# Performance work log

Hardware: AMD Instinct MI355X
Metric: run time of the kernel (lower is better)

The kernel has to match this reference:

```python
import jax, jax.numpy as jnp
import numpy as np

L, N, E, H = 1024, 8, 1024, 8


def setup_inputs() -> dict:
    key = jax.random.key(0)
    ks = jax.random.split(key, 9)
    s = 0.02
    return {
        "query": jax.random.normal(ks[0], (L, N, E), jnp.float32),
        "key": jax.random.normal(ks[1], (L, N, E), jnp.float32),
        "value": jax.random.normal(ks[2], (L, N, E), jnp.float32),
        "Wqkv": jax.random.normal(ks[3], (H, 3 * E, E), jnp.float32) * s,
        "bqkv": jax.random.normal(ks[4], (H, 3 * E), jnp.float32) * s,
        "Wo": jax.random.normal(ks[5], (H, E, E), jnp.float32) * s,
        "bo": jax.random.normal(ks[6], (H, E), jnp.float32) * s,
        "Wout": jax.random.normal(ks[7], (E, H * E), jnp.float32) * s,
        "bout": jax.random.normal(ks[8], (E,), jnp.float32) * s,
    }


def reference(query, key, value, Wqkv, bqkv, Wo, bo, Wout, bout):
    # Each of H independent single-head MultiheadAttention modules, batched over h.
    Wq, Wk, Wv = Wqkv[:, :E], Wqkv[:, E:2 * E], Wqkv[:, 2 * E:]   # [H,E,E] each
    bq, bk, bv = bqkv[:, :E], bqkv[:, E:2 * E], bqkv[:, 2 * E:]   # [H,E]
    # Projections: (L,N,E) x (H,E,E) -> (H,L,N,E)
    q = jnp.einsum('lne,hde->hlnd', query, Wq) + bq[:, None, None, :]
    k = jnp.einsum('sne,hde->hsnd', key, Wk) + bk[:, None, None, :]
    v = jnp.einsum('sne,hde->hsnd', value, Wv) + bv[:, None, None, :]
    scale = 1.0 / jnp.sqrt(jnp.asarray(E, q.dtype))  # head_dim == E since 1 head per module
    scores = jnp.einsum('hlnd,hsnd->hnls', q, k) * scale  # [H,N,L,S]
    attn_weights = jax.nn.softmax(scores, axis=-1)
    ctx = jnp.einsum('hnls,hsnd->hlnd', attn_weights, v)   # [H,L,N,E]
    head_out = jnp.einsum('hlnd,hed->hlne', ctx, Wo) + bo[:, None, None, :]
    # concat along last dim: (L,N,H*E)
    concat = jnp.transpose(head_out, (1, 2, 0, 3)).reshape(L, N, H * E)
    out = concat @ Wout.T + bout  # (L,N,E)
    return out, attn_weights  # weights: [H,N,L,S] (stack of per-head (N,L,S))
```

## Files before the change

kernel.cpp:

```cpp
#include <hip/hip_runtime.h>
#include <stdint.h>


typedef unsigned short u16;
typedef unsigned int u32;
typedef __attribute__((ext_vector_type(8))) __bf16 bf16x8;
typedef __attribute__((ext_vector_type(4))) float f32x4;
typedef __attribute__((ext_vector_type(4))) u16 u16x4;

#define DEVFN static __device__ __forceinline__

static constexpr int LQ = 1024, NN = 8, EE = 1024, HH = 8, SS = 1024;
static constexpr long LNE = (long)LQ * NN * EE;
static constexpr long MM = 1048576;

static constexpr long OF_QBF   = 0;
static constexpr long OF_KBF   = 8388608;
static constexpr long OF_VALT  = 16777216;
static constexpr long OF_F     = 25165824;
static constexpr long OF_WKT   = 33554432;
static constexpr long OF_WVT   = 41943040;
static constexpr long OF_WOT   = 50331648;
static constexpr long OF_WOUTB = 58720256;
static constexpr long OF_GT    = 67108864;
static constexpr long OF_BM    = 75497472;
static constexpr long OF_T     = 83886080;
static constexpr long OF_U     = 150994944;
static constexpr long OF_PART_F  = 109051904;
static constexpr long OF_SMALL_F = 125829120;

DEVFN u16 f2bf(float x) {
  u32 u = __builtin_bit_cast(u32, x);
  u = (u + 0x7FFFu + ((u >> 16) & 1u)) >> 16;
  return (u16)u;
}
DEVFN float bf2f(u16 x) { return __builtin_bit_cast(float, (u32)x << 16); }

DEVFN void gload16(const u16* g, u16* l) {
  __builtin_amdgcn_global_load_lds(
      (const __attribute__((address_space(1))) void*)(uintptr_t)g,
      (__attribute__((address_space(3))) void*)(uintptr_t)l, 16, 0, 0);
}

struct Cvt3P { const float* s[3]; u16* d[3]; };
__global__ __launch_bounds__(256) void k_cvt3(Cvt3P p) {
  const int z = blockIdx.y;
  const float* s = p.s[z];
  u16* d = p.d[z];
  long i = (long)blockIdx.x * 256 + threadIdx.x;
  for (; i < 2097152; i += 131072) {
    float4 v = reinterpret_cast<const float4*>(s)[i];
    u16x4 o;
    o.x = f2bf(v.x); o.y = f2bf(v.y); o.z = f2bf(v.z); o.w = f2bf(v.w);
    reinterpret_cast<u16x4*>(d)[i] = o;
  }
}

struct Tp5P { const float* s[5]; u16* d[5]; int sld[5]; long szs[5]; long dzs[5]; };
__global__ __launch_bounds__(256) void k_tp5(Tp5P p) {
  const int cfg = blockIdx.z >> 3, zz = blockIdx.z & 7;
  const float* src = p.s[cfg] + (long)zz * p.szs[cfg];
  u16* dst = p.d[cfg] + (long)zz * p.dzs[cfg];
  const int sld = p.sld[cfg];
  __shared__ float t[64][65];
  const int r = threadIdx.x >> 4, c4 = (threadIdx.x & 15) * 4;
#pragma unroll
  for (int rr = 0; rr < 64; rr += 16) {
    float4 v = *reinterpret_cast<const float4*>(
        &src[(long)(blockIdx.y * 64 + r + rr) * sld + blockIdx.x * 64 + c4]);
    t[r + rr][c4] = v.x; t[r + rr][c4 + 1] = v.y;
    t[r + rr][c4 + 2] = v.z; t[r + rr][c4 + 3] = v.w;
  }
  __syncthreads();
#pragma unroll
  for (int rr = 0; rr < 64; rr += 16) {
    u16x4 o;
    o.x = f2bf(t[c4][r + rr]);     o.y = f2bf(t[c4 + 1][r + rr]);
    o.z = f2bf(t[c4 + 2][r + rr]); o.w = f2bf(t[c4 + 3][r + rr]);
    *reinterpret_cast<u16x4*>(
        &dst[(long)(blockIdx.x * 64 + r + rr) * 1024 + blockIdx.y * 64 + c4]) = o;
  }
}

__global__ __launch_bounds__(256) void k_c(const float* __restrict__ bqkv,
                                           float* __restrict__ c) {
  const int h = blockIdx.x, t = threadIdx.x;
  float s = 0.f;
  for (int i = t; i < 1024; i += 256)
    s += bqkv[h * 3072 + i] * bqkv[h * 3072 + 1024 + i];
#pragma unroll
  for (int o = 1; o < 64; o <<= 1) s += __shfl_xor(s, o);
  __shared__ float ps[4];
  if ((t & 63) == 0) ps[t >> 6] = s;
  __syncthreads();
  if (t == 0) c[h] = ps[0] + ps[1] + ps[2] + ps[3];
}

__global__ __launch_bounds__(256) void k_ab(const float* __restrict__ Wqkv,
                                            const float* __restrict__ bqkv,
                                            float* __restrict__ ap,
                                            float* __restrict__ bp) {
  const int ec = blockIdx.x, h = blockIdx.y, dc = blockIdx.z, t = threadIdx.x;
  const int e = ec * 256 + t;
  const float* wq = Wqkv + (long)h * 3145728;
  const float* wk = wq + 1048576;
  const float* bq = bqkv + h * 3072;
  const float* bk = bq + 1024;
  float sa = 0.f, sb = 0.f;
  for (int dd = 0; dd < 128; ++dd) {
    const int d = dc * 128 + dd;
    sa += wq[(long)d * 1024 + e] * bk[d];
    sb += wk[(long)d * 1024 + e] * bq[d];
  }
  ap[dc * 8192 + h * 1024 + e] = sa;
  bp[dc * 8192 + h * 1024 + e] = sb;
}

__global__ __launch_bounds__(256) void k_red(const float* __restrict__ ap,
                                             const float* __restrict__ bp,
                                             float* __restrict__ a,
                                             float* __restrict__ b) {
  const int i = blockIdx.x * 256 + threadIdx.x;
  float sa = 0.f, sb = 0.f;
#pragma unroll
  for (int dc = 0; dc < 8; ++dc) { sa += ap[dc * 8192 + i]; sb += bp[dc * 8192 + i]; }
  a[i] = sa; b[i] = sb;
}

__global__ __launch_bounds__(256) void k_rowdot(const float* __restrict__ X,
                                                const float* __restrict__ V,
                                                const float* __restrict__ c,
                                                float* __restrict__ OUT,
                                                int addc) {
  const int wave = threadIdx.x >> 6, lane = threadIdx.x & 63;
  const int r = blockIdx.x * 4 + wave;
  const float4* xr = reinterpret_cast<const float4*>(X + (long)r * 1024);
  float acc[8];
#pragma unroll
  for (int h = 0; h < 8; ++h) acc[h] = 0.f;
#pragma unroll
  for (int it = 0; it < 4; ++it) {
    float4 q = xr[it * 64 + lane];
#pragma unroll
    for (int h = 0; h < 8; ++h) {
      float4 av = reinterpret_cast<const float4*>(V + h * 1024)[it * 64 + lane];
      acc[h] += q.x * av.x + q.y * av.y + q.z * av.z + q.w * av.w;
    }
  }
#pragma unroll
  for (int h = 0; h < 8; ++h)
#pragma unroll
    for (int o = 1; o < 64; o <<= 1) acc[h] += __shfl_xor(acc[h], o);
  if (lane == 0) {
    const int idx = r >> 3, n = r & 7;
#pragma unroll
    for (int h = 0; h < 8; ++h)
      OUT[h * 8192 + n * 1024 + idx] = acc[h] + (addc ? c[h] : 0.f);
  }
}

__global__ __launch_bounds__(256) void k_be2(const float* __restrict__ Wout,
                                             const float* __restrict__ bo,
                                             const float* __restrict__ bout,
                                             const float* __restrict__ bqkv,
                                             const u16* __restrict__ Bm,
                                             float* __restrict__ be2) {
  const int e = blockIdx.x, t = threadIdx.x;
  float s = 0.f;
  for (int i = t; i < 8192; i += 256) {
    s += Wout[(long)e * 8192 + i] * bo[i];
    const int h = i >> 10, d = i & 1023;
    s += bf2f(Bm[(long)e * 8192 + i]) * bqkv[h * 3072 + 2048 + d];
  }
#pragma unroll
  for (int o = 1; o < 64; o <<= 1) s += __shfl_xor(s, o);
  __shared__ float ps[4];
  if ((t & 63) == 0) ps[t >> 6] = s;
  __syncthreads();
  if (t == 0) be2[e] = bout[e] + ps[0] + ps[1] + ps[2] + ps[3];
}

__global__ __launch_bounds__(256) void k_combine(const float* __restrict__ p0,
                                                 const float* __restrict__ p1,
                                                 const float* __restrict__ be,
                                                 float* __restrict__ out) {
  long i = (long)blockIdx.x * 256 + threadIdx.x;
  const long st = (long)gridDim.x * 256;
  for (; i < 2097152; i += st) {
    float4 a = reinterpret_cast<const float4*>(p0)[i];
    float4 b = reinterpret_cast<const float4*>(p1)[i];
    float4 c = reinterpret_cast<const float4*>(be)[i & 255];
    float4 o = {a.x + b.x + c.x, a.y + b.y + c.y, a.z + b.z + c.z, a.w + b.w + c.w};
    reinterpret_cast<float4*>(out)[i] = o;
  }
}

__global__ __launch_bounds__(256) void k_softmax(float* __restrict__ S,
                                                 u16* __restrict__ P) {
  __shared__ float smax[4], ssum[4];
  const long row = blockIdx.x;
  float* sr = S + row * 1024;
  const int tid = threadIdx.x;
  float4 v = reinterpret_cast<const float4*>(sr)[tid];
  float m = fmaxf(fmaxf(v.x, v.y), fmaxf(v.z, v.w));
#pragma unroll
  for (int o = 1; o < 64; o <<= 1) m = fmaxf(m, __shfl_xor(m, o));
  const int wv = tid >> 6, ln = tid & 63;
  if (ln == 0) smax[wv] = m;
  __syncthreads();
  m = fmaxf(fmaxf(smax[0], smax[1]), fmaxf(smax[2], smax[3]));
  v.x = __expf(v.x - m); v.y = __expf(v.y - m);
  v.z = __expf(v.z - m); v.w = __expf(v.w - m);
  float s = v.x + v.y + v.z + v.w;
#pragma unroll
  for (int o = 1; o < 64; o <<= 1) s += __shfl_xor(s, o);
  if (ln == 0) ssum[wv] = s;
  __syncthreads();
  s = ssum[0] + ssum[1] + ssum[2] + ssum[3];
  const float inv = 1.0f / s;
  v.x *= inv; v.y *= inv; v.z *= inv; v.w *= inv;
  reinterpret_cast<float4*>(sr)[tid] = v;
  u16x4 o4;
  o4.x = f2bf(v.x); o4.y = f2bf(v.y); o4.z = f2bf(v.z); o4.w = f2bf(v.w);
  reinterpret_cast<u16x4*>(P + row * 1024)[tid] = o4;
}

struct GemmP {
  const u16* A; const u16* B;
  const float* bR; const float* bC;
  float* Cf; u16* Cb;
  int lda, ldb, ldc, K, NB;
  long sAh, sAn, sBh, sBn, sCh, sCn;
  long bRh, bRn, bCh, bCn;
  float scale;
};
struct GemmP2 { GemmP p0, p1; int split; };

template <int M0, int N0>
DEVFN void quad(f32x4 (&acc)[8][4], bf16x8 (&a)[4][2], bf16x8 (&b)[4][2]) {
#pragma unroll
  for (int mi = 0; mi < 4; ++mi)
#pragma unroll
    for (int ni = 0; ni < 2; ++ni) {
      acc[M0 + mi][N0 + ni] = __builtin_amdgcn_mfma_f32_16x16x32_bf16(
          a[mi][0], b[N0 + ni][0], acc[M0 + mi][N0 + ni], 0, 0, 0);
      acc[M0 + mi][N0 + ni] = __builtin_amdgcn_mfma_f32_16x16x32_bf16(
          a[mi][1], b[N0 + ni][1], acc[M0 + mi][N0 + ni], 0, 0, 0);
    }
}

#define BAR() asm volatile("s_barrier" ::: "memory")
#define VMCNT2() asm volatile("s_waitcnt vmcnt(2)" ::: "memory")
#define VMCNT0() asm volatile("s_waitcnt vmcnt(0)" ::: "memory")
#define SB0() __builtin_amdgcn_sched_barrier(0)

DEVFN void swz_block(int& bx, int& by, int& bz) {
  long lid = blockIdx.x + (long)gridDim.x * (blockIdx.y + (long)gridDim.y * blockIdx.z);
  const long nwg = (long)gridDim.x * gridDim.y * gridDim.z;
  long s = (nwg % 8 == 0) ? ((lid % 8) * (nwg / 8) + lid / 8) : lid;
  bx = (int)(s % gridDim.x);
  long r2 = s / gridDim.x;
  by = (int)(r2 % gridDim.y);
  bz = (int)(r2 / gridDim.y);
}

template <int HAS_BR, int HAS_BC, int OUT_F32>
DEVFN void gemm_body(const GemmP& p, int bx, int by, int bz) {
  const int h = bz / p.NB, n = bz % p.NB;
  const u16* Ab = p.A + (long)h * p.sAh + (long)n * p.sAn;
  const u16* Bb = p.B + (long)h * p.sBh + (long)n * p.sBn;
  const long coff = (long)h * p.sCh + (long)n * p.sCn;
  const int row0 = by * 256;
  const int col0 = bx * 256;

  __shared__ u16 LDSU[65536];

  const int tid = threadIdx.x;
  const int wave = tid >> 6, lane = tid & 63;
  const int wr = wave >> 2, wc = wave & 3;
  const int NT = p.K >> 6;

  f32x4 acc[8][4];
  const f32x4 zero = {0.f, 0.f, 0.f, 0.f};
#pragma unroll
  for (int i = 0; i < 8; ++i)
#pragma unroll
    for (int j = 0; j < 4; ++j) acc[i][j] = zero;

  const int swc = ((lane & 7) ^ ((lane >> 3) & 7)) * 8;
  const u16* Ag = Ab + (long)(row0 + wave * 16 + (lane >> 3)) * p.lda + swc;
  const u16* Bg = Bb + (long)(col0 + wave * 16 + (lane >> 3)) * p.ldb + swc;

  auto STAGE = [&](int hh) {
    const int kt = hh >> 2;
    if (kt < NT) {
      const int pt = hh & 3;
      const int hf = pt >> 1;
      u16* l = &LDSU[((pt & 1) ? 32768 : 0) + (kt & 1) * 16384 + hf * 8192 + wave * 1024];
      const int ld = (pt & 1) ? p.ldb : p.lda;
      const u16* g = ((pt & 1) ? Bg : Ag) + (long)hf * 128 * ld + kt * 64;
      gload16(g, l);
      gload16(g + 8L * ld, l + 512);
    }
  };

  STAGE(0); STAGE(1); STAGE(2); STAGE(3); STAGE(4);
  VMCNT2();
  BAR();

  const int rA = lane & 15;
  const int c0 = (((lane >> 4)) ^ (lane & 7)) * 8;
  const int c1 = ((4 + (lane >> 4)) ^ (lane & 7)) * 8;

  bf16x8 a[4][2], b[4][2];

  for (int t = 0; t < NT; ++t) {
    const int db = (t & 1) * 16384;
    const u16* Ar = &LDSU[db + wr * 8192 + rA * 64];
    const u16* Br = &LDSU[32768 + db + (wc >> 1) * 8192 + ((wc & 1) * 64 + rA) * 64];

#pragma unroll
    for (int mi = 0; mi < 4; ++mi) {
      a[mi][0] = *reinterpret_cast<const bf16x8*>(&Ar[mi * 1024 + c0]);
      a[mi][1] = *reinterpret_cast<const bf16x8*>(&Ar[mi * 1024 + c1]);
    }
#pragma unroll
    for (int ni = 0; ni < 2; ++ni) {
      b[ni][0] = *reinterpret_cast<const bf16x8*>(&Br[ni * 1024 + c0]);
      b[ni][1] = *reinterpret_cast<const bf16x8*>(&Br[ni * 1024 + c1]);
    }
    STAGE(4 * t + 5);
    BAR();
    SB0(); __builtin_amdgcn_s_setprio(1);
    quad<0, 0>(acc, a, b);
    __builtin_amdgcn_s_setprio(0); SB0();
    BAR();

#pragma unroll
    for (int ni = 2; ni < 4; ++ni) {
      b[ni][0] = *reinterpret_cast<const bf16x8*>(&Br[ni * 1024 + c0]);
      b[ni][1] = *reinterpret_cast<const bf16x8*>(&Br[ni * 1024 + c1]);
    }
    STAGE(4 * t + 6);
    BAR();
    SB0(); __builtin_amdgcn_s_setprio(1);
    quad<0, 2>(acc, a, b);
    __builtin_amdgcn_s_setprio(0); SB0();
    BAR();

#pragma unroll
    for (int mi = 0; mi < 4; ++mi) {
      a[mi][0] = *reinterpret_cast<const bf16x8*>(&Ar[(4 + mi) * 1024 + c0]);
      a[mi][1] = *reinterpret_cast<const bf16x8*>(&Ar[(4 + mi) * 1024 + c1]);
    }
    STAGE(4 * t + 7);
    BAR();
    SB0(); __builtin_amdgcn_s_setprio(1);
    quad<4, 0>(acc, a, b);
    __builtin_amdgcn_s_setprio(0); SB0();
    BAR();

    STAGE(4 * t + 8);
    if (t < NT - 2) { VMCNT2(); }
    else if (t == NT - 2) { VMCNT0(); }
    BAR();
    SB0(); __builtin_amdgcn_s_setprio(1);
    quad<4, 2>(acc, a, b);
    __builtin_amdgcn_s_setprio(0); SB0();
    BAR();
  }

  const int crow = (lane >> 4) * 4;
  const int ccol = lane & 15;
#pragma unroll
  for (int mi = 0; mi < 8; ++mi) {
#pragma unroll
    for (int j = 0; j < 4; ++j) {
      const int grow = row0 + wr * 128 + mi * 16 + crow + j;
#pragma unroll
      for (int ni = 0; ni < 4; ++ni) {
        const int gcol = col0 + wc * 64 + ni * 16 + ccol;
        float v = acc[mi][ni][j];
        if constexpr (HAS_BR) v += p.bR[(long)h * p.bRh + (long)n * p.bRn + grow];
        if constexpr (HAS_BC) v += p.bC[(long)h * p.bCh + (long)n * p.bCn + gcol];
        v *= p.scale;
        if constexpr (OUT_F32)
          p.Cf[coff + (long)grow * p.ldc + gcol] = v;
        else
          p.Cb[coff + (long)grow * p.ldc + gcol] = f2bf(v);
      }
    }
  }
}

template <int HAS_BR, int HAS_BC, int OUT_F32>
__global__ __launch_bounds__(512, 2) void k_gemm256(GemmP p) {
  int bx, by, bz;
  swz_block(bx, by, bz);
  gemm_body<HAS_BR, HAS_BC, OUT_F32>(p, bx, by, bz);
}

template <int HAS_BR, int HAS_BC, int OUT_F32>
__global__ __launch_bounds__(512, 2) void k_gemm256_pair(GemmP2 pp) {
  int bx, by, bz;
  swz_block(bx, by, bz);
  if (bz < pp.split)
    gemm_body<HAS_BR, HAS_BC, OUT_F32>(pp.p0, bx, by, bz);
  else
    gemm_body<HAS_BR, HAS_BC, OUT_F32>(pp.p1, bx, by, bz - pp.split);
}

extern "C" void kernel_launch(void* const* d_in, const int* in_sizes, int n_in,
                              void* d_out, int out_size, void* d_ws,
                              size_t ws_size, hipStream_t stream) {
  const float* query = (const float*)d_in[0];
  const float* key_  = (const float*)d_in[1];
  const float* value = (const float*)d_in[2];
  const float* Wqkv  = (const float*)d_in[3];
  const float* bqkv  = (const float*)d_in[4];
  const float* Wo    = (const float*)d_in[5];
  const float* bo    = (const float*)d_in[6];
  const float* Wout  = (const float*)d_in[7];
  const float* bout  = (const float*)d_in[8];

  float* out  = (float*)d_out;
  float* attn = out + LNE;

  u16* ws = (u16*)d_ws;
  u16* qbf   = ws + OF_QBF;
  u16* kbf   = ws + OF_KBF;
  u16* valT  = ws + OF_VALT;
  u16* WqT_F = ws + OF_F;
  u16* WkT   = ws + OF_WKT;
  u16* WvT   = ws + OF_WVT;
  u16* WoT   = ws + OF_WOT;
  u16* Woutb = ws + OF_WOUTB;
  u16* Gt    = ws + OF_GT;
  u16* Bm    = ws + OF_BM;
  u16* Tbuf  = ws + OF_T;
  u16* Ubuf  = ws + OF_U;
  float* part = (float*)d_ws + OF_PART_F;
  float* S    = (float*)d_ws + OF_SMALL_F;
  float* av    = S;
  float* bv2   = S + 8192;
  float* cc    = S + 16384;
  float* alpha = S + 16400;
  float* beta  = S + 81936;
  float* be2   = S + 147472;
  float* apart = S + 148496;
  float* bpart = S + 214032;

  {
    Cvt3P p;
    p.s[0] = query; p.s[1] = key_; p.s[2] = Wout;
    p.d[0] = qbf;   p.d[1] = kbf;  p.d[2] = Woutb;
    k_cvt3<<<dim3(512, 3), 256, 0, stream>>>(p);
  }
  {
    Tp5P p;
    p.s[0] = Wqkv;           p.d[0] = WqT_F; p.sld[0] = 1024; p.szs[0] = 3145728; p.dzs[0] = MM;
    p.s[1] = Wqkv + 1048576; p.d[1] = WkT;   p.sld[1] = 1024; p.szs[1] = 3145728; p.dzs[1] = MM;
    p.s[2] = Wqkv + 2097152; p.d[2] = WvT;   p.sld[2] = 1024; p.szs[2] = 3145728; p.dzs[2] = MM;
    p.s[3] = Wo;             p.d[3] = WoT;   p.sld[3] = 1024; p.szs[3] = MM;      p.dzs[3] = MM;
    p.s[4] = value;          p.d[4] = valT;  p.sld[4] = 8192; p.szs[4] = 1024;    p.dzs[4] = MM;
    k_tp5<<<dim3(16, 16, 40), 256, 0, stream>>>(p);
  }
  k_c<<<8, 256, 0, stream>>>(bqkv, cc);
  k_ab<<<dim3(4, 8, 8), 256, 0, stream>>>(Wqkv, bqkv, apart, bpart);
  k_red<<<32, 256, 0, stream>>>(apart, bpart, av, bv2);
  k_rowdot<<<2048, 256, 0, stream>>>(query, av, cc, alpha, 1);
  k_rowdot<<<2048, 256, 0, stream>>>(key_, bv2, cc, beta, 0);

  const dim3 blk(512);

  {
    GemmP g = {};
    g.A = WkT; g.lda = 1024; g.sAh = MM; g.sAn = 0;
    g.B = WqT_F; g.ldb = 1024; g.sBh = MM; g.sBn = 0;
    g.Cb = Gt; g.ldc = 1024; g.sCh = MM; g.sCn = 0;
    g.K = 1024; g.NB = 1; g.scale = 1.f;
    GemmP m = {};
    m.A = Woutb; m.lda = 8192; m.sAh = 1024; m.sAn = 0;
    m.B = WoT; m.ldb = 1024; m.sBh = MM; m.sBn = 0;
    m.Cb = Bm; m.ldc = 8192; m.sCh = 1024; m.sCn = 0;
    m.K = 1024; m.NB = 1; m.scale = 1.f;
    GemmP2 pp = {g, m, 8};
    k_gemm256_pair<0, 0, 0><<<dim3(4, 4, 16), blk, 0, stream>>>(pp);
  }
  k_be2<<<1024, 256, 0, stream>>>(Wout, bo, bout, bqkv, Bm, be2);
  {
    GemmP t = {};
    t.A = qbf; t.lda = 8192; t.sAh = 0; t.sAn = 1024;
    t.B = Gt; t.ldb = 1024; t.sBh = MM; t.sBn = 0;
    t.Cb = Tbuf; t.ldc = 8192; t.sCh = 8388608; t.sCn = 1024;
    t.K = 1024; t.NB = 8; t.scale = 1.f;
    GemmP f = {};
    f.A = Bm; f.lda = 8192; f.sAh = 1024; f.sAn = 0;
    f.B = WvT; f.ldb = 1024; f.sBh = MM; f.sBn = 0;
    f.Cb = WqT_F; f.ldc = 8192; f.sCh = 1024; f.sCn = 0;
    f.K = 1024; f.NB = 1; f.scale = 1.f;
    GemmP2 pp = {t, f, 64};
    k_gemm256_pair<0, 0, 0><<<dim3(4, 4, 72), blk, 0, stream>>>(pp);
  }
  {
    GemmP p = {};
    p.A = Tbuf; p.lda = 8192; p.sAh = 8388608; p.sAn = 1024;
    p.B = kbf; p.ldb = 8192; p.sBh = 0; p.sBn = 1024;
    p.Cf = attn; p.ldc = 1024; p.sCh = 8388608; p.sCn = 1048576;
    p.bR = alpha; p.bRh = 8192; p.bRn = 1024;
    p.bC = beta;  p.bCh = 8192; p.bCn = 1024;
    p.K = 1024; p.NB = 8; p.scale = 1.f / 32.f;
    k_gemm256<1, 1, 1><<<dim3(4, 4, 64), blk, 0, stream>>>(p);
  }
  k_softmax<<<HH * NN * LQ, 256, 0, stream>>>(attn, Tbuf);
  {
    GemmP p = {};
    p.A = Tbuf; p.lda = 1024; p.sAh = 8388608; p.sAn = 1048576;
    p.B = valT; p.ldb = 1024; p.sBh = 0; p.sBn = 1048576;
    p.Cb = Ubuf; p.ldc = 65536; p.sCh = 1024; p.sCn = 8192;
    p.K = 1024; p.NB = 8; p.scale = 1.f;
    k_gemm256<0, 0, 0><<<dim3(4, 4, 64), blk, 0, stream>>>(p);
  }
  {
    GemmP p = {};
    p.A = Ubuf; p.lda = 8192; p.sAh = 4096; p.sAn = 0;
    p.B = WqT_F; p.ldb = 8192; p.sBh = 4096; p.sBn = 0;
    p.Cf = part; p.ldc = 1024; p.sCh = 8388608; p.sCn = 0;
    p.K = 4096; p.NB = 1; p.scale = 1.f;
    k_gemm256<0, 0, 1><<<dim3(4, 32, 2), blk, 0, stream>>>(p);
  }
  k_combine<<<2048, 256, 0, stream>>>(part, part + 8388608, be2, out);
}
```

Baseline: 1.004 ms.

## Fuse score GEMM with full-row softmax and drop row-constant bias terms

```diff
diff --git a/kernel.cpp b/kernel.cpp
--- a/kernel.cpp
+++ b/kernel.cpp
@@ -25,9 +25,8 @@
 static constexpr long OF_GT    = 67108864;
 static constexpr long OF_BM    = 75497472;
 static constexpr long OF_T     = 83886080;
-static constexpr long OF_U     = 150994944;
-static constexpr long OF_PART_F  = 109051904;
-static constexpr long OF_SMALL_F = 125829120;
+static constexpr long OF_P     = 150994944;
+static constexpr long OF_SMALL_F = 109051904;
 
 DEVFN u16 f2bf(float x) {
   u32 u = __builtin_bit_cast(u32, x);
@@ -41,6 +40,13 @@
       (const __attribute__((address_space(1))) void*)(uintptr_t)g,
       (__attribute__((address_space(3))) void*)(uintptr_t)l, 16, 0, 0);
 }
+
+#define BAR() asm volatile("s_barrier" ::: "memory")
+#define VMCNT2() asm volatile("s_waitcnt vmcnt(2)" ::: "memory")
+#define VMCNT0() asm volatile("s_waitcnt vmcnt(0)" ::: "memory")
+#define VMCNT8() asm volatile("s_waitcnt vmcnt(8)" ::: "memory")
+#define VMCNT9() asm volatile("s_waitcnt vmcnt(9)" ::: "memory")
+#define SB0() __builtin_amdgcn_sched_barrier(0)
 
 struct Cvt3P { const float* s[3]; u16* d[3]; };
 __global__ __launch_bounds__(256) void k_cvt3(Cvt3P p) {
@@ -82,56 +88,32 @@
   }
 }
 
-__global__ __launch_bounds__(256) void k_c(const float* __restrict__ bqkv,
-                                           float* __restrict__ c) {
-  const int h = blockIdx.x, t = threadIdx.x;
-  float s = 0.f;
-  for (int i = t; i < 1024; i += 256)
-    s += bqkv[h * 3072 + i] * bqkv[h * 3072 + 1024 + i];
-#pragma unroll
-  for (int o = 1; o < 64; o <<= 1) s += __shfl_xor(s, o);
-  __shared__ float ps[4];
-  if ((t & 63) == 0) ps[t >> 6] = s;
-  __syncthreads();
-  if (t == 0) c[h] = ps[0] + ps[1] + ps[2] + ps[3];
-}
-
-__global__ __launch_bounds__(256) void k_ab(const float* __restrict__ Wqkv,
-                                            const float* __restrict__ bqkv,
-                                            float* __restrict__ ap,
-                                            float* __restrict__ bp) {
+__global__ __launch_bounds__(256) void k_bvec(const float* __restrict__ Wqkv,
+                                              const float* __restrict__ bqkv,
+                                              float* __restrict__ bp) {
   const int ec = blockIdx.x, h = blockIdx.y, dc = blockIdx.z, t = threadIdx.x;
   const int e = ec * 256 + t;
-  const float* wq = Wqkv + (long)h * 3145728;
-  const float* wk = wq + 1048576;
+  const float* wk = Wqkv + (long)h * 3145728 + 1048576;
   const float* bq = bqkv + h * 3072;
-  const float* bk = bq + 1024;
-  float sa = 0.f, sb = 0.f;
+  float sb = 0.f;
   for (int dd = 0; dd < 128; ++dd) {
     const int d = dc * 128 + dd;
-    sa += wq[(long)d * 1024 + e] * bk[d];
     sb += wk[(long)d * 1024 + e] * bq[d];
   }
-  ap[dc * 8192 + h * 1024 + e] = sa;
   bp[dc * 8192 + h * 1024 + e] = sb;
 }
-
-__global__ __launch_bounds__(256) void k_red(const float* __restrict__ ap,
-                                             const float* __restrict__ bp,
-                                             float* __restrict__ a,
-                                             float* __restrict__ b) {
+__global__ __launch_bounds__(256) void k_redb(const float* __restrict__ bp,
+                                              float* __restrict__ b) {
   const int i = blockIdx.x * 256 + threadIdx.x;
-  float sa = 0.f, sb = 0.f;
-#pragma unroll
-  for (int dc = 0; dc < 8; ++dc) { sa += ap[dc * 8192 + i]; sb += bp[dc * 8192 + i]; }
-  a[i] = sa; b[i] = sb;
+  float sb = 0.f;
+#pragma unroll
+  for (int dc = 0; dc < 8; ++dc) sb += bp[dc * 8192 + i];
+  b[i] = sb;
 }
 
 __global__ __launch_bounds__(256) void k_rowdot(const float* __restrict__ X,
                                                 const float* __restrict__ V,
-                                                const float* __restrict__ c,
-                                                float* __restrict__ OUT,
-                                                int addc) {
+                                                float* __restrict__ OUT) {
   const int wave = threadIdx.x >> 6, lane = threadIdx.x & 63;
   const int r = blockIdx.x * 4 + wave;
   const float4* xr = reinterpret_cast<const float4*>(X + (long)r * 1024);
@@ -154,8 +136,7 @@
   if (lane == 0) {
     const int idx = r >> 3, n = r & 7;
 #pragma unroll
-    for (int h = 0; h < 8; ++h)
-      OUT[h * 8192 + n * 1024 + idx] = acc[h] + (addc ? c[h] : 0.f);
+    for (int h = 0; h < 8; ++h) OUT[h * 8192 + n * 1024 + idx] = acc[h];
   }
 }
 
@@ -180,58 +161,28 @@
   if (t == 0) be2[e] = bout[e] + ps[0] + ps[1] + ps[2] + ps[3];
 }
 
-__global__ __launch_bounds__(256) void k_combine(const float* __restrict__ p0,
-                                                 const float* __restrict__ p1,
-                                                 const float* __restrict__ be,
-                                                 float* __restrict__ out) {
+__global__ __launch_bounds__(256) void k_combine4(const float* __restrict__ pt,
+                                                  const float* __restrict__ be,
+                                                  float* __restrict__ out) {
   long i = (long)blockIdx.x * 256 + threadIdx.x;
   const long st = (long)gridDim.x * 256;
   for (; i < 2097152; i += st) {
-    float4 a = reinterpret_cast<const float4*>(p0)[i];
-    float4 b = reinterpret_cast<const float4*>(p1)[i];
-    float4 c = reinterpret_cast<const float4*>(be)[i & 255];
-    float4 o = {a.x + b.x + c.x, a.y + b.y + c.y, a.z + b.z + c.z, a.w + b.w + c.w};
+    float4 a = reinterpret_cast<const float4*>(pt)[i];
+    float4 b = reinterpret_cast<const float4*>(pt + 8388608)[i];
+    float4 cc = reinterpret_cast<const float4*>(pt + 16777216)[i];
+    float4 d = reinterpret_cast<const float4*>(pt + 25165824)[i];
+    float4 e = reinterpret_cast<const float4*>(be)[i & 255];
+    float4 o = {a.x + b.x + cc.x + d.x + e.x, a.y + b.y + cc.y + d.y + e.y,
+                a.z + b.z + cc.z + d.z + e.z, a.w + b.w + cc.w + d.w + e.w};
     reinterpret_cast<float4*>(out)[i] = o;
   }
-}
-
-__global__ __launch_bounds__(256) void k_softmax(float* __restrict__ S,
-                                                 u16* __restrict__ P) {
-  __shared__ float smax[4], ssum[4];
-  const long row = blockIdx.x;
-  float* sr = S + row * 1024;
-  const int tid = threadIdx.x;
-  float4 v = reinterpret_cast<const float4*>(sr)[tid];
-  float m = fmaxf(fmaxf(v.x, v.y), fmaxf(v.z, v.w));
-#pragma unroll
-  for (int o = 1; o < 64; o <<= 1) m = fmaxf(m, __shfl_xor(m, o));
-  const int wv = tid >> 6, ln = tid & 63;
-  if (ln == 0) smax[wv] = m;
-  __syncthreads();
-  m = fmaxf(fmaxf(smax[0], smax[1]), fmaxf(smax[2], smax[3]));
-  v.x = __expf(v.x - m); v.y = __expf(v.y - m);
-  v.z = __expf(v.z - m); v.w = __expf(v.w - m);
-  float s = v.x + v.y + v.z + v.w;
-#pragma unroll
-  for (int o = 1; o < 64; o <<= 1) s += __shfl_xor(s, o);
-  if (ln == 0) ssum[wv] = s;
-  __syncthreads();
-  s = ssum[0] + ssum[1] + ssum[2] + ssum[3];
-  const float inv = 1.0f / s;
-  v.x *= inv; v.y *= inv; v.z *= inv; v.w *= inv;
-  reinterpret_cast<float4*>(sr)[tid] = v;
-  u16x4 o4;
-  o4.x = f2bf(v.x); o4.y = f2bf(v.y); o4.z = f2bf(v.z); o4.w = f2bf(v.w);
-  reinterpret_cast<u16x4*>(P + row * 1024)[tid] = o4;
 }
 
 struct GemmP {
   const u16* A; const u16* B;
-  const float* bR; const float* bC;
   float* Cf; u16* Cb;
   int lda, ldb, ldc, K, NB;
   long sAh, sAn, sBh, sBn, sCh, sCn;
-  long bRh, bRn, bCh, bCn;
   float scale;
 };
 struct GemmP2 { GemmP p0, p1; int split; };
@@ -248,11 +199,6 @@
           a[mi][1], b[N0 + ni][1], acc[M0 + mi][N0 + ni], 0, 0, 0);
     }
 }
-
-#define BAR() asm volatile("s_barrier" ::: "memory")
-#define VMCNT2() asm volatile("s_waitcnt vmcnt(2)" ::: "memory")
-#define VMCNT0() asm volatile("s_waitcnt vmcnt(0)" ::: "memory")
-#define SB0() __builtin_amdgcn_sched_barrier(0)
 
 DEVFN void swz_block(int& bx, int& by, int& bz) {
   long lid = blockIdx.x + (long)gridDim.x * (blockIdx.y + (long)gridDim.y * blockIdx.z);
@@ -264,7 +210,7 @@
   bz = (int)(r2 / gridDim.y);
 }
 
-template <int HAS_BR, int HAS_BC, int OUT_F32>
+template <int OUT_F32>
 DEVFN void gemm_body(const GemmP& p, int bx, int by, int bz) {
   const int h = bz / p.NB, n = bz % p.NB;
   const u16* Ab = p.A + (long)h * p.sAh + (long)n * p.sAn;
@@ -380,10 +326,7 @@
 #pragma unroll
       for (int ni = 0; ni < 4; ++ni) {
         const int gcol = col0 + wc * 64 + ni * 16 + ccol;
-        float v = acc[mi][ni][j];
-        if constexpr (HAS_BR) v += p.bR[(long)h * p.bRh + (long)n * p.bRn + grow];
-        if constexpr (HAS_BC) v += p.bC[(long)h * p.bCh + (long)n * p.bCn + gcol];
-        v *= p.scale;
+        float v = acc[mi][ni][j] * p.scale;
         if constexpr (OUT_F32)
           p.Cf[coff + (long)grow * p.ldc + gcol] = v;
         else
@@ -393,21 +336,207 @@
   }
 }
 
-template <int HAS_BR, int HAS_BC, int OUT_F32>
+template <int OUT_F32>
 __global__ __launch_bounds__(512, 2) void k_gemm256(GemmP p) {
   int bx, by, bz;
   swz_block(bx, by, bz);
-  gemm_body<HAS_BR, HAS_BC, OUT_F32>(p, bx, by, bz);
-}
-
-template <int HAS_BR, int HAS_BC, int OUT_F32>
+  gemm_body<OUT_F32>(p, bx, by, bz);
+}
+template <int OUT_F32>
 __global__ __launch_bounds__(512, 2) void k_gemm256_pair(GemmP2 pp) {
   int bx, by, bz;
   swz_block(bx, by, bz);
-  if (bz < pp.split)
-    gemm_body<HAS_BR, HAS_BC, OUT_F32>(pp.p0, bx, by, bz);
-  else
-    gemm_body<HAS_BR, HAS_BC, OUT_F32>(pp.p1, bx, by, bz - pp.split);
+  if (bz < pp.split) gemm_body<OUT_F32>(pp.p0, bx, by, bz);
+  else gemm_body<OUT_F32>(pp.p1, bx, by, bz - pp.split);
+}
+
+struct FscP {
+  const u16* T; const u16* K; const float* beta;
+  float* attn; u16* P;
+};
+__global__ __launch_bounds__(512, 2) void k_fsc(FscP p) {
+  int bx, by, bz;
+  swz_block(bx, by, bz);
+  const int h = by >> 3, n = by & 7;
+  const int row0 = bx * 64;
+
+  __shared__ u16 Abuf[2][64][64];
+  __shared__ u16 Bbuf[2][8][128][32];
+  __shared__ float red[2][64][8];
+
+  const int tid = threadIdx.x;
+  const int w = tid >> 6, lane = tid & 63;
+  const int rl = lane & 15, g = lane >> 4;
+
+  const u16* Abase = p.T + (long)h * 8388608 + n * 1024 + (long)row0 * 8192;
+  const u16* Bbase = p.K + n * 1024;
+  const float* betap = p.beta + h * 8192 + n * 1024 + w * 128 + rl;
+
+  float betv[8];
+#pragma unroll
+  for (int ni = 0; ni < 8; ++ni) betv[ni] = betap[ni * 16];
+
+  f32x4 acc[4][8];
+  const f32x4 zero = {0.f, 0.f, 0.f, 0.f};
+#pragma unroll
+  for (int mi = 0; mi < 4; ++mi)
+#pragma unroll
+    for (int ni = 0; ni < 8; ++ni) acc[mi][ni] = zero;
+
+  const u16* Bg = Bbase + (long)(w * 128 + (lane >> 2)) * 8192 +
+                  ((lane & 3) ^ ((lane >> 2) & 3)) * 8;
+  const u16* Ag = Abase + (long)(w * 8 + (lane >> 3)) * 8192 +
+                  ((lane & 7) ^ ((lane >> 3) & 7)) * 8;
+
+  auto STAGE_B = [&](int j) {
+    u16* l = &Bbuf[j & 1][w][0][0];
+    const u16* gp = Bg + (long)j * 32;
+#pragma unroll
+    for (int i = 0; i < 8; ++i) gload16(gp + (long)i * 16 * 8192, l + i * 512);
+  };
+  auto STAGE_A = [&](int pp2) {
+    gload16(Ag + (long)pp2 * 64, &Abuf[pp2 & 1][w * 8][0]);
+  };
+
+  STAGE_B(0); STAGE_A(0); STAGE_B(1); STAGE_A(1);
+
+  const int cA0 = ((g) ^ (lane & 7)) * 8;
+  const int cA1 = ((4 + g) ^ (lane & 7)) * 8;
+  const int cB = (g ^ (lane & 3)) * 8;
+
+  for (int t2 = 0; t2 < 16; ++t2) {
+    const int pb = t2 & 1;
+    VMCNT9();
+    BAR();
+    {
+      bf16x8 aF[4], bF[8];
+#pragma unroll
+      for (int mi = 0; mi < 4; ++mi)
+        aF[mi] = *reinterpret_cast<const bf16x8*>(&Abuf[pb][mi * 16 + rl][cA0]);
+#pragma unroll
+      for (int ni = 0; ni < 8; ++ni)
+        bF[ni] = *reinterpret_cast<const bf16x8*>(&Bbuf[0][w][ni * 16 + rl][cB]);
+      SB0(); __builtin_amdgcn_s_setprio(1);
+#pragma unroll
+      for (int mi = 0; mi < 4; ++mi)
+#pragma unroll
+        for (int ni = 0; ni < 8; ++ni)
+          acc[mi][ni] = __builtin_amdgcn_mfma_f32_16x16x32_bf16(
+              aF[mi], bF[ni], acc[mi][ni], 0, 0, 0);
+      __builtin_amdgcn_s_setprio(0); SB0();
+    }
+    BAR();
+    if (t2 < 15) STAGE_B(2 * t2 + 2);
+    VMCNT8();
+    BAR();
+    {
+      bf16x8 aF[4], bF[8];
+#pragma unroll
+      for (int mi = 0; mi < 4; ++mi)
+        aF[mi] = *reinterpret_cast<const bf16x8*>(&Abuf[pb][mi * 16 + rl][cA1]);
+#pragma unroll
+      for (int ni = 0; ni < 8; ++ni)
+        bF[ni] = *reinterpret_cast<const bf16x8*>(&Bbuf[1][w][ni * 16 + rl][cB]);
+      SB0(); __builtin_amdgcn_s_setprio(1);
+#pragma unroll
+      for (int mi = 0; mi < 4; ++mi)
+#pragma unroll
+        for (int ni = 0; ni < 8; ++ni)
+          acc[mi][ni] = __builtin_amdgcn_mfma_f32_16x16x32_bf16(
+              aF[mi], bF[ni], acc[mi][ni], 0, 0, 0);
+      __builtin_amdgcn_s_setprio(0); SB0();
+    }
+    BAR();
+    if (t2 < 15) STAGE_B(2 * t2 + 3);
+    if (t2 < 14) STAGE_A(t2 + 2);
+  }
+
+  float rmax[4][4];
+#pragma unroll
+  for (int mi = 0; mi < 4; ++mi)
+#pragma unroll
+    for (int j = 0; j < 4; ++j) {
+      float m = -3.0e38f;
+#pragma unroll
+      for (int ni = 0; ni < 8; ++ni) {
+        float v = (acc[mi][ni][j] + betv[ni]) * 0.03125f;
+        acc[mi][ni][j] = v;
+        m = fmaxf(m, v);
+      }
+      rmax[mi][j] = m;
+    }
+#pragma unroll
+  for (int msk = 1; msk < 16; msk <<= 1)
+#pragma unroll
+    for (int mi = 0; mi < 4; ++mi)
+#pragma unroll
+      for (int j = 0; j < 4; ++j)
+        rmax[mi][j] = fmaxf(rmax[mi][j], __shfl_xor(rmax[mi][j], msk));
+  if (rl == 0) {
+#pragma unroll
+    for (int mi = 0; mi < 4; ++mi)
+#pragma unroll
+      for (int j = 0; j < 4; ++j) red[0][mi * 16 + g * 4 + j][w] = rmax[mi][j];
+  }
+  __syncthreads();
+  float gmax[4][4];
+#pragma unroll
+  for (int mi = 0; mi < 4; ++mi)
+#pragma unroll
+    for (int j = 0; j < 4; ++j) {
+      const int row = mi * 16 + g * 4 + j;
+      float4 x = *reinterpret_cast<const float4*>(&red[0][row][0]);
+      float4 y = *reinterpret_cast<const float4*>(&red[0][row][4]);
+      gmax[mi][j] = fmaxf(fmaxf(fmaxf(x.x, x.y), fmaxf(x.z, x.w)),
+                          fmaxf(fmaxf(y.x, y.y), fmaxf(y.z, y.w)));
+    }
+  float rsum[4][4];
+#pragma unroll
+  for (int mi = 0; mi < 4; ++mi)
+#pragma unroll
+    for (int j = 0; j < 4; ++j) {
+      float s = 0.f;
+#pragma unroll
+      for (int ni = 0; ni < 8; ++ni) {
+        float e = __expf(acc[mi][ni][j] - gmax[mi][j]);
+        acc[mi][ni][j] = e;
+        s += e;
+      }
+      rsum[mi][j] = s;
+    }
+#pragma unroll
+  for (int msk = 1; msk < 16; msk <<= 1)
+#pragma unroll
+    for (int mi = 0; mi < 4; ++mi)
+#pragma unroll
+      for (int j = 0; j < 4; ++j) rsum[mi][j] += __shfl_xor(rsum[mi][j], msk);
+  if (rl == 0) {
+#pragma unroll
+    for (int mi = 0; mi < 4; ++mi)
+#pragma unroll
+      for (int j = 0; j < 4; ++j) red[1][mi * 16 + g * 4 + j][w] = rsum[mi][j];
+  }
+  __syncthreads();
+  float* attn_b = p.attn + ((long)h * 8 + n) * 1048576;
+  u16* P_b = p.P + ((long)h * 8 + n) * 1048576;
+#pragma unroll
+  for (int mi = 0; mi < 4; ++mi)
+#pragma unroll
+    for (int j = 0; j < 4; ++j) {
+      const int row = mi * 16 + g * 4 + j;
+      float4 x = *reinterpret_cast<const float4*>(&red[1][row][0]);
+      float4 y = *reinterpret_cast<const float4*>(&red[1][row][4]);
+      const float inv =
+          1.0f / (x.x + x.y + x.z + x.w + y.x + y.y + y.z + y.w);
+      float* ar = attn_b + (long)(row0 + row) * 1024 + w * 128 + rl;
+      u16* pr = P_b + (long)(row0 + row) * 1024 + w * 128 + rl;
+#pragma unroll
+      for (int ni = 0; ni < 8; ++ni) {
+        float v = acc[mi][ni][j] * inv;
+        ar[ni * 16] = v;
+        pr[ni * 16] = f2bf(v);
+      }
+    }
 }
 
 extern "C" void kernel_launch(void* const* d_in, const int* in_sizes, int n_in,
@@ -438,17 +567,13 @@
   u16* Gt    = ws + OF_GT;
   u16* Bm    = ws + OF_BM;
   u16* Tbuf  = ws + OF_T;
-  u16* Ubuf  = ws + OF_U;
-  float* part = (float*)d_ws + OF_PART_F;
-  float* S    = (float*)d_ws + OF_SMALL_F;
-  float* av    = S;
-  float* bv2   = S + 8192;
-  float* cc    = S + 16384;
-  float* alpha = S + 16400;
-  float* beta  = S + 81936;
-  float* be2   = S + 147472;
-  float* apart = S + 148496;
-  float* bpart = S + 214032;
+  u16* Pbuf  = ws + OF_P;
+  float* part = (float*)(ws + OF_P);
+  float* Sf   = (float*)d_ws + OF_SMALL_F;
+  float* beta  = Sf;
+  float* bv2   = Sf + 65536;
+  float* be2   = Sf + 73728;
+  float* bpart = Sf + 74752;
 
   {
     Cvt3P p;
@@ -465,11 +590,9 @@
     p.s[4] = value;          p.d[4] = valT;  p.sld[4] = 8192; p.szs[4] = 1024;    p.dzs[4] = MM;
     k_tp5<<<dim3(16, 16, 40), 256, 0, stream>>>(p);
   }
-  k_c<<<8, 256, 0, stream>>>(bqkv, cc);
-  k_ab<<<dim3(4, 8, 8), 256, 0, stream>>>(Wqkv, bqkv, apart, bpart);
-  k_red<<<32, 256, 0, stream>>>(apart, bpart, av, bv2);
-  k_rowdot<<<2048, 256, 0, stream>>>(query, av, cc, alpha, 1);
-  k_rowdot<<<2048, 256, 0, stream>>>(key_, bv2, cc, beta, 0);
+  k_bvec<<<dim3(4, 8, 8), 256, 0, stream>>>(Wqkv, bqkv, bpart);
+  k_redb<<<32, 256, 0, stream>>>(bpart, bv2);
+  k_rowdot<<<2048, 256, 0, stream>>>(key_, bv2, beta);
 
   const dim3 blk(512);
 
@@ -485,7 +608,7 @@
     m.Cb = Bm; m.ldc = 8192; m.sCh = 1024; m.sCn = 0;
     m.K = 1024; m.NB = 1; m.scale = 1.f;
     GemmP2 pp = {g, m, 8};
-    k_gemm256_pair<0, 0, 0><<<dim3(4, 4, 16), blk, 0, stream>>>(pp);
+    k_gemm256_pair<0><<<dim3(4, 4, 16), blk, 0, stream>>>(pp);
   }
   k_be2<<<1024, 256, 0, stream>>>(Wout, bo, bout, bqkv, Bm, be2);
   {
@@ -500,34 +623,27 @@
     f.Cb = WqT_F; f.ldc = 8192; f.sCh = 1024; f.sCn = 0;
     f.K = 1024; f.NB = 1; f.scale = 1.f;
     GemmP2 pp = {t, f, 64};
-    k_gemm256_pair<0, 0, 0><<<dim3(4, 4, 72), blk, 0, stream>>>(pp);
+    k_gemm256_pair<0><<<dim3(4, 4, 72), blk, 0, stream>>>(pp);
+  }
+  {
+    FscP p = {Tbuf, kbf, beta, attn, Pbuf};
+    k_fsc<<<dim3(16, 64), blk, 0, stream>>>(p);
   }
   {
     GemmP p = {};
-    p.A = Tbuf; p.lda = 8192; p.sAh = 8388608; p.sAn = 1024;
-    p.B = kbf; p.ldb = 8192; p.sBh = 0; p.sBn = 1024;
-    p.Cf = attn; p.ldc = 1024; p.sCh = 8388608; p.sCn = 1048576;
-    p.bR = alpha; p.bRh = 8192; p.bRn = 1024;
-    p.bC = beta;  p.bCh = 8192; p.bCn = 1024;
-    p.K = 1024; p.NB = 8; p.scale = 1.f / 32.f;
-    k_gemm256<1, 1, 1><<<dim3(4, 4, 64), blk, 0, stream>>>(p);
-  }
-  k_softmax<<<HH * NN * LQ, 256, 0, stream>>>(attn, Tbuf);
+    p.A = Pbuf; p.lda = 1024; p.sAh = 8388608; p.sAn = 1048576;
+    p.B = valT; p.ldb = 1024; p.sBh = 0; p.sBn = 1048576;
+    p.Cb = Tbuf; p.ldc = 65536; p.sCh = 1024; p.sCn = 8192;
+    p.K = 1024; p.NB = 8; p.scale = 1.f;
+    k_gemm256<0><<<dim3(4, 4, 64), blk, 0, stream>>>(p);
+  }
   {
     GemmP p = {};
-    p.A = Tbuf; p.lda = 1024; p.sAh = 8388608; p.sAn = 1048576;
-    p.B = valT; p.ldb = 1024; p.sBh = 0; p.sBn = 1048576;
-    p.Cb = Ubuf; p.ldc = 65536; p.sCh = 1024; p.sCn = 8192;
-    p.K = 1024; p.NB = 8; p.scale = 1.f;
-    k_gemm256<0, 0, 0><<<dim3(4, 4, 64), blk, 0, stream>>>(p);
-  }
-  {
-    GemmP p = {};
-    p.A = Ubuf; p.lda = 8192; p.sAh = 4096; p.sAn = 0;
-    p.B = WqT_F; p.ldb = 8192; p.sBh = 4096; p.sBn = 0;
+    p.A = Tbuf; p.lda = 8192; p.sAh = 2048; p.sAn = 0;
+    p.B = WqT_F; p.ldb = 8192; p.sBh = 2048; p.sBn = 0;
     p.Cf = part; p.ldc = 1024; p.sCh = 8388608; p.sCn = 0;
-    p.K = 4096; p.NB = 1; p.scale = 1.f;
-    k_gemm256<0, 0, 1><<<dim3(4, 32, 2), blk, 0, stream>>>(p);
-  }
-  k_combine<<<2048, 256, 0, stream>>>(part, part + 8388608, be2, out);
-}
+    p.K = 2048; p.NB = 1; p.scale = 1.f;
+    k_gemm256<1><<<dim3(4, 32, 4), blk, 0, stream>>>(p);
+  }
+  k_combine4<<<2048, 256, 0, stream>>>(part, be2, out);
+}
```

Result: no change. 991.6 us (-1.2%).
